# Optimization experiments

Measured on AMD Instinct MI355X. Metric: run time of the kernel, lower is better.

Reference implementation:

```python
import jax, jax.numpy as jnp
import numpy as np

B, T, D, K = 8, 4096, 1024, 3


def setup_inputs() -> dict:
    key = jax.random.key(0)
    k0, k1, k2 = jax.random.split(key, 3)
    x = jax.random.normal(k0, (B, T, D), dtype=jnp.float32)
    lim = 1.0 / np.sqrt(D)
    Wv = jax.random.uniform(k1, (D, D), dtype=jnp.float32, minval=-lim, maxval=lim)
    bv = jnp.zeros((D,), dtype=jnp.float32)
    Wo = jax.random.uniform(k2, (D, D), dtype=jnp.float32, minval=-lim, maxval=lim)
    bo = jnp.zeros((D,), dtype=jnp.float32)
    neighbor_weights = jnp.ones((K,), dtype=jnp.float32) / K
    return {"x": x, "Wv": Wv, "bv": bv, "Wo": Wo, "bo": bo,
            "neighbor_weights": neighbor_weights}


def reference(x, Wv, bv, Wo, bo, neighbor_weights):
    # x: [B, T, D]; faithful translation of the unfold -> Linear -> weighted-sum chain
    k = neighbor_weights.shape[0]
    pad = k // 2
    t = x.shape[1]
    # replicate padding along T (torch F.pad mode='replicate')
    xp = jnp.pad(x, ((0, 0), (pad, pad), (0, 0)), mode='edge')  # [B, T+2*pad, D]
    # sliding windows: [B, T, K, D] (small fixed K loop, not a data-dim loop)
    windows = jnp.stack([xp[:, i:i + t, :] for i in range(k)], axis=2)
    # value projection applied per window element (nn.Linear: x @ W.T + b)
    v = jnp.einsum('btkd,ed->btke', windows, Wv) + bv  # [B, T, K, D]
    # fixed-weight neighbor average
    attended = jnp.einsum('btkd,k->btd', v, neighbor_weights)  # [B, T, D]
    # output projection
    return jnp.einsum('btd,ed->bte', attended, Wo) + bo
```

## Files before the change

kernel.cpp:

```cpp
#include <hip/hip_runtime.h>
#include <stdint.h>
#include <stddef.h>

typedef _Float16 f16_t;
typedef _Float16 f16x4 __attribute__((ext_vector_type(4)));
typedef _Float16 f16x8 __attribute__((ext_vector_type(8)));
typedef float f32x4 __attribute__((ext_vector_type(4)));
typedef float f32x8 __attribute__((ext_vector_type(8)));

#define AS_G __attribute__((address_space(1)))
#define AS_L __attribute__((address_space(3)))

__device__ __forceinline__ void gload_lds16(const void* g, void* l) {
  __builtin_amdgcn_global_load_lds((AS_G void*)g, (AS_L void*)l, 16, 0, 0);
}

#define FENCE() asm volatile("" ::: "memory")
#define BARX()                            \
  do {                                    \
    FENCE();                              \
    __builtin_amdgcn_s_barrier();         \
    FENCE();                              \
  } while (0)
#define VMCNT(n) asm volatile("s_waitcnt vmcnt(" #n ")" ::: "memory")


__global__ __launch_bounds__(256) void prep_fused_kernel(
    const float* __restrict__ X, const float* __restrict__ Wo,
    const float* __restrict__ Wv, const float* __restrict__ bv,
    const float* __restrict__ bo, const float* __restrict__ nw, int Kw,
    f16_t* __restrict__ Xavg, f16_t* __restrict__ WcT, float* __restrict__ bc) {
  __shared__ __align__(16) f16_t sA[128 * 32];
  __shared__ __align__(16) float sWv[32 * 132];
  __shared__ float smem[256];
  const int b = blockIdx.x;
  const int tid = threadIdx.x;

  if (b < 4096) {
    const int T = 4096, D = 1024;
    const int base = b * 8;
    const int bb = (base >> 12) << 12;
    const int be = bb + T - 1;
    const int half = tid >> 7;
    const int c8 = (tid & 127) * 8;
    const float w0 = nw[0], w1 = nw[1], w2 = nw[2];
#pragma unroll
    for (int g = 0; g < 4; ++g) {
      const int r = base + 2 * g + half;
      const int rm = (r > bb) ? r - 1 : bb;
      const int rp = (r < be) ? r + 1 : be;
      f32x8 a = *(const f32x8*)(X + (size_t)rm * D + c8);
      f32x8 v = *(const f32x8*)(X + (size_t)r * D + c8);
      f32x8 c = *(const f32x8*)(X + (size_t)rp * D + c8);
      f32x8 y = w0 * a + w1 * v + w2 * c;
      f16x8 o;
#pragma unroll
      for (int e = 0; e < 8; ++e) o[e] = (f16_t)y[e];
      *(f16x8*)(Xavg + (size_t)r * D + c8) = o;
    }
  } else if (b < 4160) {
    constexpr int K = 1024, NN = 1024;
    const int bid = b - 4096;
    const int mt = bid & 7, nt = bid >> 3;
    const int m0 = mt << 7, n0 = nt << 7;
    const int l = tid & 63, w = tid >> 6;
    const int wr = w >> 1, wc = w & 1;
    const int ka = (l >> 4) << 3;
    const int ar = (wr << 6) + (l & 15);
    const int br = (wc << 6) + (l & 15);

    f32x4 acc[4][4];
#pragma unroll
    for (int i = 0; i < 4; ++i)
#pragma unroll
      for (int j = 0; j < 4; ++j) acc[i][j] = f32x4{0.f, 0.f, 0.f, 0.f};

    for (int kt = 0; kt < (K >> 5); ++kt) {
      const int kb = kt << 5;
#pragma unroll
      for (int i = 0; i < 2; ++i) {
        const int u = tid + i * 256;
        const int row = u >> 2, ch = u & 3;
        f32x8 v = *(const f32x8*)(Wo + (size_t)(m0 + row) * K + kb + ch * 8);
        f16x8 h;
#pragma unroll
        for (int e = 0; e < 8; ++e) h[e] = (f16_t)v[e];
        *(f16x8*)(sA + row * 32 + ch * 8) = h;
      }
#pragma unroll
      for (int i = 0; i < 4; ++i) {
        const int u = tid + i * 256;
        const int k = u >> 5, c4 = u & 31;
        f32x4 v = *(const f32x4*)(Wv + (size_t)(kb + k) * NN + n0 + c4 * 4);
        *(f32x4*)(sWv + k * 132 + c4 * 4) = v;
      }
      __syncthreads();
      f16x8 af[4], bfr[4];
#pragma unroll
      for (int m = 0; m < 4; ++m) af[m] = *(const f16x8*)(sA + (ar + (m << 4)) * 32 + ka);
#pragma unroll
      for (int n = 0; n < 4; ++n) {
#pragma unroll
        for (int e = 0; e < 8; ++e)
          bfr[n][e] = (f16_t)sWv[(ka + e) * 132 + br + (n << 4)];
      }
#pragma unroll
      for (int m = 0; m < 4; ++m)
#pragma unroll
        for (int n = 0; n < 4; ++n)
          acc[m][n] = __builtin_amdgcn_mfma_f32_16x16x32_f16(af[m], bfr[n], acc[m][n], 0, 0, 0);
      __syncthreads();
    }

    const int orow = (l >> 4) << 2;
    const int ocol = l & 15;
#pragma unroll
    for (int n = 0; n < 4; ++n) {
      const int gn = n0 + (wc << 6) + (n << 4) + ocol;
#pragma unroll
      for (int m = 0; m < 4; ++m) {
        const int gm = m0 + (wr << 6) + (m << 4) + orow;
#pragma unroll
        for (int j = 0; j < 4; ++j)
          WcT[(size_t)(gm + j) * NN + gn] = (f16_t)acc[m][n][j];
      }
    }
  } else {
    const int e = b - 4160;
    float sw = 0.f;
    for (int k = 0; k < Kw; ++k) sw += nw[k];
    float p = 0.f;
    for (int d = tid; d < 1024; d += 256) p += Wo[(size_t)e * 1024 + d] * bv[d];
    smem[tid] = p;
    __syncthreads();
    for (int s = 128; s > 0; s >>= 1) {
      if (tid < s) smem[tid] += smem[tid + s];
      __syncthreads();
    }
    if (tid == 0) bc[e] = sw * smem[0] + bo[e];
  }
}


__device__ __forceinline__ void stage256(const f16_t* __restrict__ g, int K,
                                         f16_t* ldsOp, int w, int l) {
#pragma unroll
  for (int i = 0; i < 2; ++i) {
    const int f = i * 512 + w * 64 + l;
    const int row = f >> 2;
    const int ch = f & 3;
    const int col = (((ch ^ ((row >> 1) & 3))) << 3);
    gload_lds16(g + (size_t)row * K + col, ldsOp + i * 4096 + w * 512);
  }
}

__global__ __launch_bounds__(512, 2) void gemm256_kernel(const f16_t* __restrict__ A,
                                                         const f16_t* __restrict__ Bt,
                                                         float* __restrict__ C,
                                                         const float* __restrict__ bias,
                                                         int M, int N, int K) {
  __shared__ __align__(16) f16_t lds[4 * 16384];
  const int tid = threadIdx.x;
  const int l = tid & 63;
  const int w = tid >> 6;
  const int wr = w >> 2;
  const int wc = w & 3;
  const int lr = l & 15;
  const int q = l >> 4;

  const int cpx = (int)gridDim.x >> 3;
  const int swzb = ((int)blockIdx.x & 7) * cpx + ((int)blockIdx.x >> 3);
  const int nNT = N >> 8;
  const int mt = swzb / nNT;
  const int nt = swzb % nNT;
  const int m0 = mt << 8;
  const int n0 = nt << 8;

  const f16_t* Apanel = A + (size_t)m0 * K;
  const f16_t* Bpanel = Bt + (size_t)n0 * K;
  const int sw = (q ^ ((lr >> 1) & 3)) << 3;

  f32x4 acc[8][4];
#pragma unroll
  for (int m = 0; m < 8; ++m)
#pragma unroll
    for (int n = 0; n < 4; ++n) acc[m][n] = f32x4{0.f, 0.f, 0.f, 0.f};

  const int nK = K >> 5;

  for (int t = 0; t < 3; ++t) {
    f16_t* buf = lds + (t & 3) * 16384;
    stage256(Apanel + (t << 5), K, buf, w, l);
    stage256(Bpanel + (t << 5), K, buf + 8192, w, l);
  }
  VMCNT(8);
  BARX();

  for (int t = 0; t < nK; ++t) {
    f16_t* sA = lds + (t & 3) * 16384;
    f16_t* sB = sA + 8192;

    {
      const int tn = (t + 3) < nK ? (t + 3) : (nK - 1);
      f16_t* nbuf = lds + ((t + 3) & 3) * 16384;
      stage256(Apanel + ((size_t)tn << 5), K, nbuf, w, l);
      stage256(Bpanel + ((size_t)tn << 5), K, nbuf + 8192, w, l);
    }

    f16x8 bf[4], af[4], ag[4];
#pragma unroll
    for (int n = 0; n < 4; ++n)
      bf[n] = *(const f16x8*)(sB + (((wc << 6) + (n << 4) + lr) << 5) + sw);
#pragma unroll
    for (int m = 0; m < 4; ++m)
      af[m] = *(const f16x8*)(sA + (((wr << 7) + (m << 4) + lr) << 5) + sw);
#pragma unroll
    for (int m = 0; m < 4; ++m)
      ag[m] = *(const f16x8*)(sA + (((wr << 7) + 64 + (m << 4) + lr) << 5) + sw);

    __builtin_amdgcn_s_setprio(1);
#pragma unroll
    for (int m = 0; m < 4; ++m)
#pragma unroll
      for (int n = 0; n < 4; ++n)
        acc[m][n] = __builtin_amdgcn_mfma_f32_16x16x32_f16(af[m], bf[n], acc[m][n], 0, 0, 0);
#pragma unroll
    for (int m = 0; m < 4; ++m)
#pragma unroll
      for (int n = 0; n < 4; ++n)
        acc[m + 4][n] = __builtin_amdgcn_mfma_f32_16x16x32_f16(ag[m], bf[n], acc[m + 4][n], 0, 0, 0);
    __builtin_amdgcn_s_setprio(0);

    VMCNT(8);
    BARX();
  }

  float bs[4];
#pragma unroll
  for (int n = 0; n < 4; ++n) bs[n] = bias[n0 + (wc << 6) + (n << 4) + lr];
#pragma unroll
  for (int m = 0; m < 8; ++m) {
    const int gm = m0 + (wr << 7) + (m << 4) + (q << 2);
#pragma unroll
    for (int j = 0; j < 4; ++j) {
      float* Crow = C + (size_t)(gm + j) * N + n0 + (wc << 6) + lr;
#pragma unroll
      for (int n = 0; n < 4; ++n) Crow[n << 4] = acc[m][n][j] + bs[n];
    }
  }
}


extern "C" void kernel_launch(void* const* d_in, const int* in_sizes, int n_in,
                              void* d_out, int out_size, void* d_ws, size_t ws_size,
                              hipStream_t stream) {
  const float* x = (const float*)d_in[0];
  const float* Wv = (const float*)d_in[1];
  const float* bv = (const float*)d_in[2];
  const float* Wo = (const float*)d_in[3];
  const float* bo = (const float*)d_in[4];
  const float* nw = (const float*)d_in[5];
  float* out = (float*)d_out;

  char* ws = (char*)d_ws;
  f16_t* WcT  = (f16_t*)(ws + (4u << 20));
  float* bc   = (float*)(ws + (6u << 20));
  f16_t* Xavg = (f16_t*)(ws + (8u << 20));

  prep_fused_kernel<<<dim3(5184), dim3(256), 0, stream>>>(
      x, Wo, Wv, bv, bo, nw, in_sizes[5], Xavg, WcT, bc);
  gemm256_kernel<<<dim3(512), dim3(512), 0, stream>>>(
      Xavg, WcT, out, bc, 32768, 1024, 1024);
}
```

Baseline: 161.4 us.

## Reorder prep blocks, reuse rows in stencil, transpose Wv tile in LDS

The fused prep kernel now schedules the weight-fold GEMM and bias blocks first, so the long-running GEMM tiles start early instead of trailing the stencil blocks. The stencil blocks now walk 8 consecutive rows per thread with a sliding register window, so each X row is loaded once rather than three times. The Wv tile is stored transposed in LDS so B fragments are read with vector loads instead of eight strided scalar reads. The transposed store is a scalar scatter and may cause LDS bank conflicts.

```diff
diff --git a/kernel.cpp b/kernel.cpp
--- a/kernel.cpp
+++ b/kernel.cpp
@@ -31,43 +31,23 @@
     const float* __restrict__ bo, const float* __restrict__ nw, int Kw,
     f16_t* __restrict__ Xavg, f16_t* __restrict__ WcT, float* __restrict__ bc) {
   __shared__ __align__(16) f16_t sA[128 * 32];
-  __shared__ __align__(16) float sWv[32 * 132];
+  __shared__ __align__(16) float sWvT[128 * 36];
   __shared__ float smem[256];
   const int b = blockIdx.x;
   const int tid = threadIdx.x;
 
-  if (b < 4096) {
-    const int T = 4096, D = 1024;
-    const int base = b * 8;
-    const int bb = (base >> 12) << 12;
-    const int be = bb + T - 1;
-    const int half = tid >> 7;
-    const int c8 = (tid & 127) * 8;
-    const float w0 = nw[0], w1 = nw[1], w2 = nw[2];
-#pragma unroll
-    for (int g = 0; g < 4; ++g) {
-      const int r = base + 2 * g + half;
-      const int rm = (r > bb) ? r - 1 : bb;
-      const int rp = (r < be) ? r + 1 : be;
-      f32x8 a = *(const f32x8*)(X + (size_t)rm * D + c8);
-      f32x8 v = *(const f32x8*)(X + (size_t)r * D + c8);
-      f32x8 c = *(const f32x8*)(X + (size_t)rp * D + c8);
-      f32x8 y = w0 * a + w1 * v + w2 * c;
-      f16x8 o;
-#pragma unroll
-      for (int e = 0; e < 8; ++e) o[e] = (f16_t)y[e];
-      *(f16x8*)(Xavg + (size_t)r * D + c8) = o;
-    }
-  } else if (b < 4160) {
+  if (b < 64) {
     constexpr int K = 1024, NN = 1024;
-    const int bid = b - 4096;
-    const int mt = bid & 7, nt = bid >> 3;
+    const int mt = b & 7, nt = b >> 3;
     const int m0 = mt << 7, n0 = nt << 7;
     const int l = tid & 63, w = tid >> 6;
     const int wr = w >> 1, wc = w & 1;
-    const int ka = (l >> 4) << 3;
+    const int q = l >> 4;
+    const int ka = q << 3;
     const int ar = (wr << 6) + (l & 15);
     const int br = (wc << 6) + (l & 15);
+    const int kS = tid >> 3;
+    const int cS = (tid & 7) << 4;
 
     f32x4 acc[4][4];
 #pragma unroll
@@ -88,11 +68,10 @@
         *(f16x8*)(sA + row * 32 + ch * 8) = h;
       }
 #pragma unroll
-      for (int i = 0; i < 4; ++i) {
-        const int u = tid + i * 256;
-        const int k = u >> 5, c4 = u & 31;
-        f32x4 v = *(const f32x4*)(Wv + (size_t)(kb + k) * NN + n0 + c4 * 4);
-        *(f32x4*)(sWv + k * 132 + c4 * 4) = v;
+      for (int j = 0; j < 4; ++j) {
+        f32x4 v = *(const f32x4*)(Wv + (size_t)(kb + kS) * NN + n0 + cS + 4 * j);
+#pragma unroll
+        for (int i = 0; i < 4; ++i) sWvT[(cS + 4 * j + i) * 36 + kS] = v[i];
       }
       __syncthreads();
       f16x8 af[4], bfr[4];
@@ -100,9 +79,13 @@
       for (int m = 0; m < 4; ++m) af[m] = *(const f16x8*)(sA + (ar + (m << 4)) * 32 + ka);
 #pragma unroll
       for (int n = 0; n < 4; ++n) {
-#pragma unroll
-        for (int e = 0; e < 8; ++e)
-          bfr[n][e] = (f16_t)sWv[(ka + e) * 132 + br + (n << 4)];
+        f32x4 v0 = *(const f32x4*)(sWvT + (br + (n << 4)) * 36 + ka);
+        f32x4 v1 = *(const f32x4*)(sWvT + (br + (n << 4)) * 36 + ka + 4);
+#pragma unroll
+        for (int e = 0; e < 4; ++e) {
+          bfr[n][e] = (f16_t)v0[e];
+          bfr[n][e + 4] = (f16_t)v1[e];
+        }
       }
 #pragma unroll
       for (int m = 0; m < 4; ++m)
@@ -112,7 +95,7 @@
       __syncthreads();
     }
 
-    const int orow = (l >> 4) << 2;
+    const int orow = q << 2;
     const int ocol = l & 15;
 #pragma unroll
     for (int n = 0; n < 4; ++n) {
@@ -125,8 +108,8 @@
           WcT[(size_t)(gm + j) * NN + gn] = (f16_t)acc[m][n][j];
       }
     }
-  } else {
-    const int e = b - 4160;
+  } else if (b < 1088) {
+    const int e = b - 64;
     float sw = 0.f;
     for (int k = 0; k < Kw; ++k) sw += nw[k];
     float p = 0.f;
@@ -138,6 +121,28 @@
       __syncthreads();
     }
     if (tid == 0) bc[e] = sw * smem[0] + bo[e];
+  } else {
+    const int T = 4096, D = 1024;
+    const int base = (b - 1088) * 8;
+    const int t0 = base & (T - 1);
+    const int col = tid * 4;
+    const float w0 = nw[0], w1 = nw[1], w2 = nw[2];
+    const float* xb = X + (size_t)base * D + col;
+    f32x4 va = *(const f32x4*)(xb + (t0 == 0 ? 0 : -D));
+    f32x4 vb = *(const f32x4*)(xb);
+    f16_t* ob = Xavg + (size_t)base * D + col;
+#pragma unroll
+    for (int g = 0; g < 8; ++g) {
+      f32x4 vc;
+      if (t0 + g == T - 1) vc = vb;
+      else vc = *(const f32x4*)(xb + (size_t)(g + 1) * D);
+      f32x4 y = w0 * va + w1 * vb + w2 * vc;
+      f16x4 o;
+      o.x = (f16_t)y.x; o.y = (f16_t)y.y; o.z = (f16_t)y.z; o.w = (f16_t)y.w;
+      *(f16x4*)(ob + (size_t)g * D) = o;
+      va = vb;
+      vb = vc;
+    }
   }
 }
 
```

Result: faster. 145.1 us (-10.1%).
